# Optimization experiments

Measured on AMD Instinct MI355X. Metric: run time of the kernel, lower is better.

The kernel has to match this reference:

```python
import jax, jax.numpy as jnp
import numpy as np

ENT_N = 100000  # entity vocab (relation rows live inside this table, as in the source)
REL_N = 237
DIM = 128
N = 16384       # batch of triples
EPS = 1e-12     # F.normalize default eps


def _l2norm(x, axis=-1):
    n = jnp.linalg.norm(x, axis=axis, keepdims=True)
    return x / jnp.maximum(n, EPS)


def setup_inputs() -> dict:
    key = jax.random.key(0)
    k1, k2, k3, k4 = jax.random.split(key, 4)
    ent_emb = jax.random.normal(k1, (ENT_N, DIM), dtype=jnp.float32)
    h_ids = jax.random.randint(k2, (N,), 0, ENT_N)
    r_typ = jax.random.randint(k3, (N,), 0, REL_N)
    t_ids = jax.random.randint(k4, (N,), 0, ENT_N)
    return {"ent_emb": ent_emb, "h_ids": h_ids, "r_typ": r_typ, "t_ids": t_ids}


def reference(ent_emb, h_ids, r_typ, t_ids):
    d = ent_emb.shape[1]
    h = _l2norm(ent_emb[h_ids])           # [n, d]
    t = _l2norm(ent_emb[t_ids])           # [n, d]
    # The torch loop looks up ent_emb[r_typ*d + k] for k in range(d); gather
    # the whole relation block at once instead of d tiny lookups + cat.
    r_idx = r_typ[:, None] * d + jnp.arange(d)  # [n, d]
    R = ent_emb[r_idx]                     # [n, d, d]; row k = relation vec k
    prod = jnp.einsum('nd,nkd->nk', h, R)  # [n, d]
    prod = _l2norm(prod)
    return jnp.linalg.norm(prod - t, axis=1)  # [n]
```

## Files before the change

kernel.cpp:

```cpp
#include <hip/hip_runtime.h>

#define RELS 237
#define DIM 128
#define CH 32
#define MAXCHUNK 742
#define PREPB 64
#define MAGIC 0x5EEDF00D
#define EPS 1e-12f

typedef __attribute__((ext_vector_type(8))) short bf16x8;
typedef __attribute__((ext_vector_type(4))) float f32x4;


__device__ __forceinline__ unsigned short f2bf(float f) {
    unsigned int u = __float_as_uint(f);
    u = (u + 0x7fffu + ((u >> 16) & 1u)) >> 16;
    return (unsigned short)u;
}

__global__ __launch_bounds__(256) void k_fused(
    const float* __restrict__ ent,
    const int*   __restrict__ r_typ,
    const int*   __restrict__ h_ids,
    const int*   __restrict__ t_ids,
    int*         __restrict__ ws,
    unsigned short* __restrict__ Rc,
    int n)
{
    const int tid = threadIdx.x;

    if (blockIdx.x < RELS) {
        const int r = blockIdx.x;
        const float* src = ent + ((long)r << 14);
        unsigned short* dst = Rc + ((long)r << 14);
        #pragma unroll
        for (int s = 0; s < 8; ++s) {
            int idx = s * 256 + tid;
            int c  = idx & 15;
            int q  = (idx >> 4) & 3;
            int ks = (idx >> 6) & 3;
            int nt = idx >> 8;
            const float* sp = src + (nt * 16 + c) * 128 + ks * 32 + q * 8;
            float4 v0 = *(const float4*)sp;
            float4 v1 = *(const float4*)(sp + 4);
            uint4 wv;
            wv.x = f2bf(v0.x) | ((unsigned)f2bf(v0.y) << 16);
            wv.y = f2bf(v0.z) | ((unsigned)f2bf(v0.w) << 16);
            wv.z = f2bf(v1.x) | ((unsigned)f2bf(v1.y) << 16);
            wv.w = f2bf(v1.z) | ((unsigned)f2bf(v1.w) << 16);
            *(uint4*)(dst + (long)idx * 8) = wv;
        }
        return;
    }

    const int b = blockIdx.x - RELS;
    __shared__ int hist[256];
    __shared__ int scn[256];
    __shared__ int offsL[256];
    __shared__ int pbL[256];
    __shared__ int cursL[256];
    hist[tid] = 0;
    cursL[tid] = 0;
    __syncthreads();

    for (int i = b * 256 + tid; i < n; i += PREPB * 256)
        atomicAdd(&hist[r_typ[i]], 1);
    __syncthreads();
    ws[4096 + b * 256 + tid] = hist[tid];
    __threadfence();
    __syncthreads();
    if (tid == 0) atomicExch(&ws[2048 + b], MAGIC);

    if (tid < PREPB)
        while (atomicAdd(&ws[2048 + tid], 0) != MAGIC) __builtin_amdgcn_s_sleep(2);
    __syncthreads();

    int tot = 0, pref = 0;
    for (int bb = 0; bb < PREPB; ++bb) {
        int v = atomicAdd(&ws[4096 + bb * 256 + tid], 0);
        if (bb < b) pref += v;
        tot += v;
    }
    scn[tid] = tot; __syncthreads();
    #pragma unroll
    for (int off = 1; off < 256; off <<= 1) {
        int v = (tid >= off) ? scn[tid - off] : 0;
        __syncthreads();
        scn[tid] += v; __syncthreads();
    }
    const int offs = scn[tid] - tot;
    offsL[tid] = offs;
    pbL[tid]   = pref;
    __syncthreads();

    if (b == 0) {
        const int nch = (tot + CH - 1) >> 5;
        scn[tid] = nch; __syncthreads();
        #pragma unroll
        for (int off = 1; off < 256; off <<= 1) {
            int v = (tid >= off) ? scn[tid - off] : 0;
            __syncthreads();
            scn[tid] += v; __syncthreads();
        }
        const int choff = scn[tid] - nch;
        if (tid == 255) ws[1000] = scn[255];
        for (int j = 0; j < nch; ++j) {
            int len = tot - j * CH; if (len > CH) len = CH;
            ws[1024 + choff + j] = (tid << 20) | ((offs + j * CH) << 6) | len;
        }
    }

    for (int i = b * 256 + tid; i < n; i += PREPB * 256) {
        int rr  = r_typ[i];
        int pos = offsL[rr] + pbL[rr] + atomicAdd(&cursL[rr], 1);
        ws[32768 + pos] = i;
        ws[49152 + pos] = h_ids[i];
        ws[65536 + pos] = t_ids[i];
    }
}

__global__ __launch_bounds__(256, 4) void relgemm(
    const float*          __restrict__ ent,
    const unsigned short* __restrict__ Rc,
    const int*            __restrict__ ws,
    float*                __restrict__ out)
{
    __shared__ char smem[17152];
    unsigned short* Hb = (unsigned short*)smem;
    float* Pp  = (float*)smem;
    int*  sidx = (int*)(smem + 16896);
    int*  tRow = (int*)(smem + 17024);

    const int cid = blockIdx.x;
    if (cid >= ws[1000]) return;
    const int e    = ws[1024 + cid];
    const int r    = e >> 20;
    const int base = (e >> 6) & 16383;
    const int len  = e & 63;

    const int tid  = threadIdx.x;
    const int lane = tid & 63;
    const int w    = tid >> 6;

    if (tid < CH) {
        int tc = tid < len ? tid : len - 1;
        sidx[tid] = ws[32768 + base + tc];
        tRow[tid] = ws[65536 + base + tc];
    }

    #pragma unroll
    for (int s = 0; s < 4; ++s) {
        int g = s * 256 + tid;
        int trow = g >> 5, c4 = g & 31;
        int tc = trow < len ? trow : len - 1;
        int hid = ws[49152 + base + tc];
        float4 v = ((const float4*)ent)[((long)hid << 5) + c4];
        ushort4 bb; bb.x = f2bf(v.x); bb.y = f2bf(v.y); bb.z = f2bf(v.z); bb.w = f2bf(v.w);
        *(ushort4*)(Hb + trow * 136 + c4 * 4) = bb;
    }
    __syncthreads();

    const int q = lane >> 4, c = lane & 15;
    const unsigned short* A0p = Hb + c * 136 + q * 8;
    const unsigned short* A1p = Hb + (c + 16) * 136 + q * 8;
    const unsigned short* Bp  = Rc + ((long)r << 14) + w * 4096 + q * 128 + c * 8;

    f32x4 a00 = {0.f,0.f,0.f,0.f}, a01 = a00, a10 = a00, a11 = a00;
    #pragma unroll
    for (int ks = 0; ks < 4; ++ks) {
        bf16x8 B0 = *(const bf16x8*)(Bp + ks * 512);
        bf16x8 B1 = *(const bf16x8*)(Bp + 2048 + ks * 512);
        bf16x8 A0 = *(const bf16x8*)(A0p + ks * 32);
        bf16x8 A1 = *(const bf16x8*)(A1p + ks * 32);
        a00 = __builtin_amdgcn_mfma_f32_16x16x32_bf16(A0, B0, a00, 0, 0, 0);
        a01 = __builtin_amdgcn_mfma_f32_16x16x32_bf16(A0, B1, a01, 0, 0, 0);
        a10 = __builtin_amdgcn_mfma_f32_16x16x32_bf16(A1, B0, a10, 0, 0, 0);
        a11 = __builtin_amdgcn_mfma_f32_16x16x32_bf16(A1, B1, a11, 0, 0, 0);
    }
    __syncthreads();

    #pragma unroll
    for (int reg = 0; reg < 4; ++reg) {
        int m0 = q * 4 + reg;
        Pp[m0 * 132        + w * 32      + c] = a00[reg];
        Pp[m0 * 132        + w * 32 + 16 + c] = a01[reg];
        Pp[(m0 + 16) * 132 + w * 32      + c] = a10[reg];
        Pp[(m0 + 16) * 132 + w * 32 + 16 + c] = a11[reg];
    }
    __syncthreads();

    float p0v[8], p1v[8], t0v[8], t1v[8];
    #pragma unroll
    for (int tt = 0; tt < 8; ++tt) {
        int t = w * 8 + tt;
        int trow = tRow[t];
        const float* tv = ent + ((long)trow << 7);
        t0v[tt] = tv[lane];
        t1v[tt] = tv[lane + 64];
        p0v[tt] = Pp[t * 132 + lane];
        p1v[tt] = Pp[t * 132 + 64 + lane];
    }
    #pragma unroll
    for (int tt = 0; tt < 8; ++tt) {
        int t   = w * 8 + tt;
        float p0 = p0v[tt], p1 = p1v[tt];
        float tv0 = t0v[tt], tv1 = t1v[tt];
        float sp  = p0 * p0 + p1 * p1;
        float st  = tv0 * tv0 + tv1 * tv1;
        float spt = p0 * tv0 + p1 * tv1;
        #pragma unroll
        for (int m = 32; m >= 1; m >>= 1) {
            sp  += __shfl_xor(sp,  m, 64);
            st  += __shfl_xor(st,  m, 64);
            spt += __shfl_xor(spt, m, 64);
        }
        if (lane == 0 && t < len) {
            float npn = fmaxf(sqrtf(sp), EPS);
            float ntn = fmaxf(sqrtf(st), EPS);
            float v   = 2.0f - 2.0f * (spt / (npn * ntn));
            out[sidx[t]] = sqrtf(fmaxf(v, 0.0f));
        }
    }
}

extern "C" void kernel_launch(void* const* d_in, const int* in_sizes, int n_in,
                              void* d_out, int out_size, void* d_ws, size_t ws_size,
                              hipStream_t stream) {
    const float* ent   = (const float*)d_in[0];
    const int*   h_ids = (const int*)d_in[1];
    const int*   r_typ = (const int*)d_in[2];
    const int*   t_ids = (const int*)d_in[3];
    float* out = (float*)d_out;
    int*   ws  = (int*)d_ws;
    unsigned short* Rc = (unsigned short*)(ws + 81920);
    const int n = in_sizes[1];

    hipLaunchKernelGGL(k_fused, dim3(RELS + PREPB), dim3(256), 0, stream,
                       ent, r_typ, h_ids, t_ids, ws, Rc, n);
    hipLaunchKernelGGL(relgemm, dim3(MAXCHUNK),     dim3(256), 0, stream,
                       ent, Rc, ws, out);
}
```

Before: 114.9 us.

## Fuse bucketing and relation GEMM into one per-relation kernel with LDS-resident weights

Replaces the two-kernel pipeline (global histogram/scatter with cross-block spin barrier, then chunked GEMM) with a single kernel where each of two blocks per relation scans the whole r_typ array, builds its own index list in shared memory, converts the relation matrix to bf16 once into LDS, and loops over its 32-triple chunks. This removes a kernel launch, the inter-block spin synchronisation and the global workspace round-trips. In exchange, every block rescans all r_typ entries twice, LDS use per block grows to about 58 KB (lower occupancy), and the list is capped at 2048 entries per relation, which silently drops triples beyond that cap.

```diff
diff --git a/kernel.cpp b/kernel.cpp
--- a/kernel.cpp
+++ b/kernel.cpp
@@ -1,16 +1,14 @@
 #include <hip/hip_runtime.h>
 
 #define RELS 237
+#define SPLIT 2
 #define DIM 128
 #define CH 32
-#define MAXCHUNK 742
-#define PREPB 64
-#define MAGIC 0x5EEDF00D
+#define LISTCAP 2048
 #define EPS 1e-12f
 
 typedef __attribute__((ext_vector_type(8))) short bf16x8;
 typedef __attribute__((ext_vector_type(4))) float f32x4;
-
 
 __device__ __forceinline__ unsigned short f2bf(float f) {
     unsigned int u = __float_as_uint(f);
@@ -18,207 +16,166 @@
     return (unsigned short)u;
 }
 
-__global__ __launch_bounds__(256) void k_fused(
+__global__ __launch_bounds__(256) void relkern(
     const float* __restrict__ ent,
+    const int*   __restrict__ h_ids,
     const int*   __restrict__ r_typ,
-    const int*   __restrict__ h_ids,
     const int*   __restrict__ t_ids,
-    int*         __restrict__ ws,
-    unsigned short* __restrict__ Rc,
+    float*       __restrict__ out,
     int n)
 {
-    const int tid = threadIdx.x;
+    __shared__ unsigned short Bf[16384];
+    __shared__ int list[LISTCAP];
+    __shared__ int scn[256];
+    __shared__ char smem[17152];
+    unsigned short* Hb = (unsigned short*)smem;
+    float* Pp  = (float*)smem;
+    int*  sidx = (int*)(smem + 16896);
+    int*  tRow = (int*)(smem + 17024);
 
-    if (blockIdx.x < RELS) {
-        const int r = blockIdx.x;
-        const float* src = ent + ((long)r << 14);
-        unsigned short* dst = Rc + ((long)r << 14);
-        #pragma unroll
-        for (int s = 0; s < 8; ++s) {
-            int idx = s * 256 + tid;
-            int c  = idx & 15;
-            int q  = (idx >> 4) & 3;
-            int ks = (idx >> 6) & 3;
-            int nt = idx >> 8;
-            const float* sp = src + (nt * 16 + c) * 128 + ks * 32 + q * 8;
-            float4 v0 = *(const float4*)sp;
-            float4 v1 = *(const float4*)(sp + 4);
-            uint4 wv;
-            wv.x = f2bf(v0.x) | ((unsigned)f2bf(v0.y) << 16);
-            wv.y = f2bf(v0.z) | ((unsigned)f2bf(v0.w) << 16);
-            wv.z = f2bf(v1.x) | ((unsigned)f2bf(v1.y) << 16);
-            wv.w = f2bf(v1.z) | ((unsigned)f2bf(v1.w) << 16);
-            *(uint4*)(dst + (long)idx * 8) = wv;
-        }
-        return;
+    const int r    = blockIdx.x >> 1;
+    const int half = blockIdx.x & 1;
+    const int tid  = threadIdx.x;
+    const int lane = tid & 63;
+    const int w    = tid >> 6;
+
+    const int n4 = n >> 2;
+    int mycnt = 0;
+    for (int i4 = tid; i4 < n4; i4 += 256) {
+        int4 v = ((const int4*)r_typ)[i4];
+        mycnt += (v.x == r) + (v.y == r) + (v.z == r) + (v.w == r);
     }
+    for (int i = (n4 << 2) + tid; i < n; i += 256)
+        mycnt += (r_typ[i] == r);
 
-    const int b = blockIdx.x - RELS;
-    __shared__ int hist[256];
-    __shared__ int scn[256];
-    __shared__ int offsL[256];
-    __shared__ int pbL[256];
-    __shared__ int cursL[256];
-    hist[tid] = 0;
-    cursL[tid] = 0;
-    __syncthreads();
-
-    for (int i = b * 256 + tid; i < n; i += PREPB * 256)
-        atomicAdd(&hist[r_typ[i]], 1);
-    __syncthreads();
-    ws[4096 + b * 256 + tid] = hist[tid];
-    __threadfence();
-    __syncthreads();
-    if (tid == 0) atomicExch(&ws[2048 + b], MAGIC);
-
-    if (tid < PREPB)
-        while (atomicAdd(&ws[2048 + tid], 0) != MAGIC) __builtin_amdgcn_s_sleep(2);
-    __syncthreads();
-
-    int tot = 0, pref = 0;
-    for (int bb = 0; bb < PREPB; ++bb) {
-        int v = atomicAdd(&ws[4096 + bb * 256 + tid], 0);
-        if (bb < b) pref += v;
-        tot += v;
-    }
-    scn[tid] = tot; __syncthreads();
+    scn[tid] = mycnt; __syncthreads();
     #pragma unroll
     for (int off = 1; off < 256; off <<= 1) {
         int v = (tid >= off) ? scn[tid - off] : 0;
         __syncthreads();
         scn[tid] += v; __syncthreads();
     }
-    const int offs = scn[tid] - tot;
-    offsL[tid] = offs;
-    pbL[tid]   = pref;
+    int pos = scn[tid] - mycnt;
+    int cnt = scn[255];
+    if (cnt > LISTCAP) cnt = LISTCAP;
+
+    for (int i4 = tid; i4 < n4; i4 += 256) {
+        int4 v = ((const int4*)r_typ)[i4];
+        int i = i4 << 2;
+        if (v.x == r && pos < LISTCAP) list[pos++] = i;
+        if (v.y == r && pos < LISTCAP) list[pos++] = i + 1;
+        if (v.z == r && pos < LISTCAP) list[pos++] = i + 2;
+        if (v.w == r && pos < LISTCAP) list[pos++] = i + 3;
+    }
+    for (int i = (n4 << 2) + tid; i < n; i += 256)
+        if (r_typ[i] == r && pos < LISTCAP) list[pos++] = i;
     __syncthreads();
 
-    if (b == 0) {
-        const int nch = (tot + CH - 1) >> 5;
-        scn[tid] = nch; __syncthreads();
-        #pragma unroll
-        for (int off = 1; off < 256; off <<= 1) {
-            int v = (tid >= off) ? scn[tid - off] : 0;
-            __syncthreads();
-            scn[tid] += v; __syncthreads();
-        }
-        const int choff = scn[tid] - nch;
-        if (tid == 255) ws[1000] = scn[255];
-        for (int j = 0; j < nch; ++j) {
-            int len = tot - j * CH; if (len > CH) len = CH;
-            ws[1024 + choff + j] = (tid << 20) | ((offs + j * CH) << 6) | len;
-        }
+    const int nch = (cnt + CH - 1) >> 5;
+    if (half >= nch) return;
+
+    const float* src = ent + ((long)r << 14);
+    #pragma unroll
+    for (int s = 0; s < 8; ++s) {
+        int idx = s * 256 + tid;
+        int c  = idx & 15;
+        int q  = (idx >> 4) & 3;
+        int ks = (idx >> 6) & 3;
+        int nt = idx >> 8;
+        const float* sp = src + (nt * 16 + c) * 128 + ks * 32 + q * 8;
+        float4 v0 = *(const float4*)sp;
+        float4 v1 = *(const float4*)(sp + 4);
+        uint4 wv;
+        wv.x = f2bf(v0.x) | ((unsigned)f2bf(v0.y) << 16);
+        wv.y = f2bf(v0.z) | ((unsigned)f2bf(v0.w) << 16);
+        wv.z = f2bf(v1.x) | ((unsigned)f2bf(v1.y) << 16);
+        wv.w = f2bf(v1.z) | ((unsigned)f2bf(v1.w) << 16);
+        *(uint4*)(Bf + (long)idx * 8) = wv;
     }
-
-    for (int i = b * 256 + tid; i < n; i += PREPB * 256) {
-        int rr  = r_typ[i];
-        int pos = offsL[rr] + pbL[rr] + atomicAdd(&cursL[rr], 1);
-        ws[32768 + pos] = i;
-        ws[49152 + pos] = h_ids[i];
-        ws[65536 + pos] = t_ids[i];
-    }
-}
-
-__global__ __launch_bounds__(256, 4) void relgemm(
-    const float*          __restrict__ ent,
-    const unsigned short* __restrict__ Rc,
-    const int*            __restrict__ ws,
-    float*                __restrict__ out)
-{
-    __shared__ char smem[17152];
-    unsigned short* Hb = (unsigned short*)smem;
-    float* Pp  = (float*)smem;
-    int*  sidx = (int*)(smem + 16896);
-    int*  tRow = (int*)(smem + 17024);
-
-    const int cid = blockIdx.x;
-    if (cid >= ws[1000]) return;
-    const int e    = ws[1024 + cid];
-    const int r    = e >> 20;
-    const int base = (e >> 6) & 16383;
-    const int len  = e & 63;
-
-    const int tid  = threadIdx.x;
-    const int lane = tid & 63;
-    const int w    = tid >> 6;
-
-    if (tid < CH) {
-        int tc = tid < len ? tid : len - 1;
-        sidx[tid] = ws[32768 + base + tc];
-        tRow[tid] = ws[65536 + base + tc];
-    }
-
-    #pragma unroll
-    for (int s = 0; s < 4; ++s) {
-        int g = s * 256 + tid;
-        int trow = g >> 5, c4 = g & 31;
-        int tc = trow < len ? trow : len - 1;
-        int hid = ws[49152 + base + tc];
-        float4 v = ((const float4*)ent)[((long)hid << 5) + c4];
-        ushort4 bb; bb.x = f2bf(v.x); bb.y = f2bf(v.y); bb.z = f2bf(v.z); bb.w = f2bf(v.w);
-        *(ushort4*)(Hb + trow * 136 + c4 * 4) = bb;
-    }
-    __syncthreads();
 
     const int q = lane >> 4, c = lane & 15;
     const unsigned short* A0p = Hb + c * 136 + q * 8;
     const unsigned short* A1p = Hb + (c + 16) * 136 + q * 8;
-    const unsigned short* Bp  = Rc + ((long)r << 14) + w * 4096 + q * 128 + c * 8;
+    const unsigned short* Bp  = Bf + w * 4096 + q * 128 + c * 8;
 
-    f32x4 a00 = {0.f,0.f,0.f,0.f}, a01 = a00, a10 = a00, a11 = a00;
-    #pragma unroll
-    for (int ks = 0; ks < 4; ++ks) {
-        bf16x8 B0 = *(const bf16x8*)(Bp + ks * 512);
-        bf16x8 B1 = *(const bf16x8*)(Bp + 2048 + ks * 512);
-        bf16x8 A0 = *(const bf16x8*)(A0p + ks * 32);
-        bf16x8 A1 = *(const bf16x8*)(A1p + ks * 32);
-        a00 = __builtin_amdgcn_mfma_f32_16x16x32_bf16(A0, B0, a00, 0, 0, 0);
-        a01 = __builtin_amdgcn_mfma_f32_16x16x32_bf16(A0, B1, a01, 0, 0, 0);
-        a10 = __builtin_amdgcn_mfma_f32_16x16x32_bf16(A1, B0, a10, 0, 0, 0);
-        a11 = __builtin_amdgcn_mfma_f32_16x16x32_bf16(A1, B1, a11, 0, 0, 0);
-    }
-    __syncthreads();
+    for (int j = half; j < nch; j += SPLIT) {
+        const int base = j * CH;
+        int len = cnt - base; if (len > CH) len = CH;
 
-    #pragma unroll
-    for (int reg = 0; reg < 4; ++reg) {
-        int m0 = q * 4 + reg;
-        Pp[m0 * 132        + w * 32      + c] = a00[reg];
-        Pp[m0 * 132        + w * 32 + 16 + c] = a01[reg];
-        Pp[(m0 + 16) * 132 + w * 32      + c] = a10[reg];
-        Pp[(m0 + 16) * 132 + w * 32 + 16 + c] = a11[reg];
-    }
-    __syncthreads();
+        __syncthreads();
+        if (tid < CH) {
+            int tc = tid < len ? tid : len - 1;
+            int t3 = list[base + tc];
+            sidx[tid] = t3;
+            tRow[tid] = t_ids[t3];
+        }
+        #pragma unroll
+        for (int s = 0; s < 4; ++s) {
+            int g = s * 256 + tid;
+            int trow = g >> 5, c4 = g & 31;
+            int tc = trow < len ? trow : len - 1;
+            int hid = h_ids[list[base + tc]];
+            float4 v = ((const float4*)ent)[((long)hid << 5) + c4];
+            ushort4 bb; bb.x = f2bf(v.x); bb.y = f2bf(v.y); bb.z = f2bf(v.z); bb.w = f2bf(v.w);
+            *(ushort4*)(Hb + trow * 136 + c4 * 4) = bb;
+        }
+        __syncthreads();
 
-    float p0v[8], p1v[8], t0v[8], t1v[8];
-    #pragma unroll
-    for (int tt = 0; tt < 8; ++tt) {
-        int t = w * 8 + tt;
-        int trow = tRow[t];
-        const float* tv = ent + ((long)trow << 7);
-        t0v[tt] = tv[lane];
-        t1v[tt] = tv[lane + 64];
-        p0v[tt] = Pp[t * 132 + lane];
-        p1v[tt] = Pp[t * 132 + 64 + lane];
-    }
-    #pragma unroll
-    for (int tt = 0; tt < 8; ++tt) {
-        int t   = w * 8 + tt;
-        float p0 = p0v[tt], p1 = p1v[tt];
-        float tv0 = t0v[tt], tv1 = t1v[tt];
-        float sp  = p0 * p0 + p1 * p1;
-        float st  = tv0 * tv0 + tv1 * tv1;
-        float spt = p0 * tv0 + p1 * tv1;
+        f32x4 a00 = {0.f,0.f,0.f,0.f}, a01 = a00, a10 = a00, a11 = a00;
         #pragma unroll
-        for (int m = 32; m >= 1; m >>= 1) {
-            sp  += __shfl_xor(sp,  m, 64);
-            st  += __shfl_xor(st,  m, 64);
-            spt += __shfl_xor(spt, m, 64);
+        for (int ks = 0; ks < 4; ++ks) {
+            bf16x8 B0 = *(const bf16x8*)(Bp + ks * 512);
+            bf16x8 B1 = *(const bf16x8*)(Bp + 2048 + ks * 512);
+            bf16x8 A0 = *(const bf16x8*)(A0p + ks * 32);
+            bf16x8 A1 = *(const bf16x8*)(A1p + ks * 32);
+            a00 = __builtin_amdgcn_mfma_f32_16x16x32_bf16(A0, B0, a00, 0, 0, 0);
+            a01 = __builtin_amdgcn_mfma_f32_16x16x32_bf16(A0, B1, a01, 0, 0, 0);
+            a10 = __builtin_amdgcn_mfma_f32_16x16x32_bf16(A1, B0, a10, 0, 0, 0);
+            a11 = __builtin_amdgcn_mfma_f32_16x16x32_bf16(A1, B1, a11, 0, 0, 0);
         }
-        if (lane == 0 && t < len) {
-            float npn = fmaxf(sqrtf(sp), EPS);
-            float ntn = fmaxf(sqrtf(st), EPS);
-            float v   = 2.0f - 2.0f * (spt / (npn * ntn));
-            out[sidx[t]] = sqrtf(fmaxf(v, 0.0f));
+        __syncthreads();
+
+        #pragma unroll
+        for (int reg = 0; reg < 4; ++reg) {
+            int m0 = q * 4 + reg;
+            Pp[m0 * 132        + w * 32      + c] = a00[reg];
+            Pp[m0 * 132        + w * 32 + 16 + c] = a01[reg];
+            Pp[(m0 + 16) * 132 + w * 32      + c] = a10[reg];
+            Pp[(m0 + 16) * 132 + w * 32 + 16 + c] = a11[reg];
+        }
+        __syncthreads();
+
+        float p0v[8], p1v[8], t0v[8], t1v[8];
+        #pragma unroll
+        for (int tt = 0; tt < 8; ++tt) {
+            int t = w * 8 + tt;
+            int trow = tRow[t];
+            const float* tv = ent + ((long)trow << 7);
+            t0v[tt] = tv[lane];
+            t1v[tt] = tv[lane + 64];
+            p0v[tt] = Pp[t * 132 + lane];
+            p1v[tt] = Pp[t * 132 + 64 + lane];
+        }
+        #pragma unroll
+        for (int tt = 0; tt < 8; ++tt) {
+            int t   = w * 8 + tt;
+            float p0 = p0v[tt], p1 = p1v[tt];
+            float tv0 = t0v[tt], tv1 = t1v[tt];
+            float sp  = p0 * p0 + p1 * p1;
+            float st  = tv0 * tv0 + tv1 * tv1;
+            float spt = p0 * tv0 + p1 * tv1;
+            #pragma unroll
+            for (int m = 32; m >= 1; m >>= 1) {
+                sp  += __shfl_xor(sp,  m, 64);
+                st  += __shfl_xor(st,  m, 64);
+                spt += __shfl_xor(spt, m, 64);
+            }
+            if (lane == 0 && t < len) {
+                float npn = fmaxf(sqrtf(sp), EPS);
+                float ntn = fmaxf(sqrtf(st), EPS);
+                float v   = 2.0f - 2.0f * (spt / (npn * ntn));
+                out[sidx[t]] = sqrtf(fmaxf(v, 0.0f));
+            }
         }
     }
 }
@@ -231,12 +188,8 @@
     const int*   r_typ = (const int*)d_in[2];
     const int*   t_ids = (const int*)d_in[3];
     float* out = (float*)d_out;
-    int*   ws  = (int*)d_ws;
-    unsigned short* Rc = (unsigned short*)(ws + 81920);
     const int n = in_sizes[1];
 
-    hipLaunchKernelGGL(k_fused, dim3(RELS + PREPB), dim3(256), 0, stream,
-                       ent, r_typ, h_ids, t_ids, ws, Rc, n);
-    hipLaunchKernelGGL(relgemm, dim3(MAXCHUNK),     dim3(256), 0, stream,
-                       ent, Rc, ws, out);
+    hipLaunchKernelGGL(relkern, dim3(RELS * SPLIT), dim3(256), 0, stream,
+                       ent, h_ids, r_typ, t_ids, out, n);
 }
```

Result: faster. 105.6 us (-8.1%).
